# Kernel optimization log

Measured on AMD Instinct MI355X. Metric: run time of the kernel, lower is better.

## Reference

```python
import jax, jax.numpy as jnp
import numpy as np

B, K, L, D, H = 8, 64, 4096, 1024, 16
HD = D // H
SCALE = HD ** -0.5


def setup_inputs() -> dict:
    key = jax.random.key(0)
    ks = jax.random.split(key, 7)
    return {
        "query": jax.random.normal(ks[0], (B, K, D), jnp.float32),
        "key": jax.random.normal(ks[1], (B, L, D), jnp.float32),
        "value": jax.random.normal(ks[2], (B, L, D), jnp.float32),
        "Wq": jax.random.normal(ks[3], (D, D), jnp.float32) * (D ** -0.5),
        "Wk": jax.random.normal(ks[4], (D, D), jnp.float32) * (D ** -0.5),
        "Wv": jax.random.normal(ks[5], (D, D), jnp.float32) * (D ** -0.5),
        "Wo": jax.random.normal(ks[6], (D, D), jnp.float32) * (D ** -0.5),
        "bo": jnp.zeros((D,), jnp.float32),
    }


def reference(query, key, value, Wq, Wk, Wv, Wo, bo):
    # torch Linear: y = x @ W.T; split heads -> [B,H,len,HD]
    q = jnp.einsum('bkd,ed->bke', query, Wq).reshape(B, K, H, HD).transpose(0, 2, 1, 3)
    k = jnp.einsum('bld,ed->ble', key, Wk).reshape(B, L, H, HD).transpose(0, 2, 1, 3)
    v = jnp.einsum('bld,ed->ble', value, Wv).reshape(B, L, H, HD).transpose(0, 2, 1, 3)
    dots = jnp.einsum('bhkc,bhlc->bhkl', q, k) * SCALE  # [B,H,K,L]
    attn = jax.nn.softmax(dots, axis=-2)               # softmax over query (slot) dim
    attn = attn / (attn.sum(axis=-1, keepdims=True) + 1e-8)  # renormalize over keys
    out = jnp.einsum('bhkl,bhlc->bhkc', attn, v)       # [B,H,K,HD]
    out = out.transpose(0, 2, 1, 3).reshape(B, K, D)
    out = jnp.einsum('bkd,ed->bke', out, Wo) + bo
    return out, attn
```

## Files before the change

### kernel.cpp

```cpp
#include <hip/hip_runtime.h>
#include <hip/hip_bf16.h>

#define B_   8
#define KS_  64
#define L_   4096
#define D_   1024
#define H_   16
#define HD_  64
#define SCALE_ 0.125f

typedef __attribute__((ext_vector_type(8))) short short8;
typedef __attribute__((ext_vector_type(8))) unsigned short ushort8;
typedef __attribute__((ext_vector_type(4))) unsigned short ushort4v;
typedef __attribute__((ext_vector_type(4))) float f32x4;

__device__ __forceinline__ unsigned short f2b(float f) {
  union { float f; unsigned u; } v; v.f = f;
  unsigned r = v.u + 0x7fffu + ((v.u >> 16) & 1u);
  return (unsigned short)(r >> 16);
}

typedef const __attribute__((address_space(1))) void gas_void;
typedef __attribute__((address_space(3))) void las_void;
__device__ __forceinline__ void gl2lds16(const void* g, void* l) {
  __builtin_amdgcn_global_load_lds((gas_void*)g, (las_void*)l, 16, 0, 0);
}

__device__ __forceinline__ void bar() {
  asm volatile("" ::: "memory");
  __builtin_amdgcn_s_barrier();
  asm volatile("" ::: "memory");
}
__device__ __forceinline__ void vm4() {
  asm volatile("s_waitcnt vmcnt(4)" ::: "memory");
}

__global__ __launch_bounds__(256) void wcvt(const float* __restrict__ wq,
                                            const float* __restrict__ wk,
                                            const float* __restrict__ wv,
                                            const float* __restrict__ wo,
                                            const float* __restrict__ query,
                                            unsigned short* __restrict__ wout,
                                            unsigned short* __restrict__ qout) {
  int i = blockIdx.x * 256 + threadIdx.x;
  const float* src;
  unsigned short* dst;
  int off;
  if (i < (4 << 18)) {
    int seg = i >> 18;
    off = (i & 0x3ffff) << 2;
    src = (seg == 0) ? wq : (seg == 1) ? wk : (seg == 2) ? wv : wo;
    dst = wout + ((size_t)seg << 20);
  } else {
    off = (i - (4 << 18)) << 2;
    src = query;
    dst = qout;
  }
  f32x4 v = *(const f32x4*)(src + off);
  ushort4v o;
#pragma unroll
  for (int j = 0; j < 4; ++j) o[j] = f2b(v[j]);
  *(ushort4v*)(dst + off) = o;
}

__global__ __launch_bounds__(256) void cvt1(const float* __restrict__ src,
                                            unsigned short* __restrict__ dst,
                                            int nunits) {
  const int stride = gridDim.x * 256;
  for (int i = blockIdx.x * 256 + threadIdx.x; i < nunits; i += stride) {
    const f32x4* p = (const f32x4*)(src + (size_t)i * 8);
    f32x4 a = __builtin_nontemporal_load(p);
    f32x4 b = __builtin_nontemporal_load(p + 1);
    ushort8 o;
#pragma unroll
    for (int j = 0; j < 4; ++j) { o[j] = f2b(a[j]); o[j + 4] = f2b(b[j]); }
    *(ushort8*)(dst + (size_t)i * 8) = o;
  }
}

__global__ __launch_bounds__(512, 2) void gemm256(const unsigned short* __restrict__ A,
                                                  const unsigned short* __restrict__ W,
                                                  unsigned short* __restrict__ C) {
  __shared__ __align__(16) char smem[131072];
  const int tid = threadIdx.x, lane = tid & 63, w = tid >> 6;
  const int g = lane >> 4, c15 = lane & 15;
  const int wm = w >> 2, wn = w & 3;

  const int swz = (blockIdx.x & 7) * 64 + (blockIdx.x >> 3);
  const long m0 = (long)(swz >> 2) * 256;
  const int  n0 = (swz & 3) * 256;

  const int srow = w * 16 + (lane >> 2);
  const int cswz = (lane & 3) ^ ((lane >> 3) & 3);
  const unsigned short* a_sr = A + (m0 + srow) * 1024 + cswz * 8;
  const unsigned short* b_sr = W + (long)(n0 + srow) * 1024 + cswz * 8;
  const int rswz = (g ^ ((c15 >> 1) & 3)) << 4;
  const int aoff = (wm * 128 + c15) * 64 + rswz;
  const int boff = 65536 + (wn * 64 + c15) * 64 + rswz;

  f32x4 acc[8][4] = {};
  short8 af[8], bf[2];

  auto STAGE_A = [&](int d, int kh, int tk) {
    char* dst = smem + d * 32768 + kh * 16384 + w * 1024;
    const unsigned short* src = a_sr + tk * 64 + kh * 32;
    gl2lds16(src,          dst);
    gl2lds16(src + 131072, dst + 8192);
  };
  auto STAGE_B = [&](int d, int kh, int tk) {
    char* dst = smem + 65536 + d * 32768 + kh * 16384 + w * 1024;
    const unsigned short* src = b_sr + tk * 64 + kh * 32;
    gl2lds16(src,          dst);
    gl2lds16(src + 131072, dst + 8192);
  };
  auto LDA = [&](int d, int ks) {
    const char* base = smem + d * 32768 + ks * 16384 + aoff;
#pragma unroll
    for (int m = 0; m < 8; ++m) af[m] = *(const short8*)(base + m * 1024);
  };
  auto LDB = [&](int d, int ks, int nh) {
    const char* base = smem + d * 32768 + ks * 16384 + boff + nh * 2048;
    bf[0] = *(const short8*)(base);
    bf[1] = *(const short8*)(base + 1024);
  };
  auto MM = [&](int nh) {
    __builtin_amdgcn_s_setprio(1);
#pragma unroll
    for (int n2 = 0; n2 < 2; ++n2)
#pragma unroll
      for (int m = 0; m < 8; ++m)
        acc[m][nh * 2 + n2] =
            __builtin_amdgcn_mfma_f32_16x16x32_bf16(af[m], bf[n2], acc[m][nh * 2 + n2], 0, 0, 0);
    __builtin_amdgcn_s_setprio(0);
  };

  STAGE_A(0, 0, 0); STAGE_B(0, 0, 0); STAGE_A(0, 1, 0); STAGE_B(0, 1, 0);
  vm4();
  bar();

#pragma unroll 1
  for (int tk = 0; tk < 16; tk += 2) {
    const bool more = (tk + 2 < 16);
    LDA(0, 0); LDB(0, 0, 0); STAGE_A(1, 0, tk + 1);          bar(); MM(0); bar();
    LDB(0, 0, 1);            STAGE_B(1, 0, tk + 1);  vm4();  bar(); MM(1); bar();
    LDA(0, 1); LDB(0, 1, 0); STAGE_A(1, 1, tk + 1);          bar(); MM(0); bar();
    LDB(0, 1, 1);            STAGE_B(1, 1, tk + 1);  vm4();  bar(); MM(1); bar();
    LDA(1, 0); LDB(1, 0, 0); if (more) STAGE_A(0, 0, tk + 2);        bar(); MM(0); bar();
    LDB(1, 0, 1);            if (more) STAGE_B(0, 0, tk + 2); vm4(); bar(); MM(1); bar();
    LDA(1, 1); LDB(1, 1, 0); if (more) STAGE_A(0, 1, tk + 2);        bar(); MM(0); bar();
    LDB(1, 1, 1);            if (more) STAGE_B(0, 1, tk + 2); vm4(); bar(); MM(1); bar();
  }

  unsigned short* cl = (unsigned short*)smem;
#pragma unroll
  for (int m = 0; m < 8; ++m)
#pragma unroll
    for (int n = 0; n < 4; ++n)
#pragma unroll
      for (int r = 0; r < 4; ++r)
        cl[(wm * 128 + m * 16 + g * 4 + r) * 256 + wn * 64 + n * 16 + c15] =
            f2b(acc[m][n][r]);
  __syncthreads();
  const int row = tid >> 1, half = tid & 1;
  unsigned short*       dst = C + (m0 + row) * 1024 + n0 + half * 128;
  const unsigned short* sl  = cl + row * 256 + half * 128;
#pragma unroll
  for (int i = 0; i < 16; ++i)
    *(ushort8*)(dst + i * 8) = *(const ushort8*)(sl + i * 8);
}

template <bool OUT_F32B>
__global__ __launch_bounds__(256) void gemm_bf16(const unsigned short* __restrict__ A,
                                                 const unsigned short* __restrict__ W,
                                                 void* __restrict__ Cp,
                                                 const float* __restrict__ bias) {
  __shared__ __align__(16) char smem[34816];
  const int tid = threadIdx.x, lane = tid & 63, wv = tid >> 6;
  const int g = lane >> 4, c15 = lane & 15;
  const int wm = wv >> 1, wn = wv & 1;

  const int nwg = gridDim.x;
  const int swz = (blockIdx.x & 7) * (nwg >> 3) + (blockIdx.x >> 3);
  const long m0 = (long)(swz >> 3) * 128;
  const int  n0 = (swz & 7) * 128;

  const int srow = lane >> 2, scol = (lane & 3) * 8;
  const unsigned short* a_src = A + (m0 + srow) * 1024 + scol;
  const unsigned short* b_src = W + (long)(n0 + srow) * 1024 + scol;

  f32x4 acc[4][4] = {};

  auto stage = [&](int buf, int kt) {
    unsigned short* al = (unsigned short*)(smem + buf * 8192);
    unsigned short* bl = (unsigned short*)(smem + 16384 + buf * 8192);
#pragma unroll
    for (int q = 0; q < 2; ++q) {
      const int rbase = q * 64 + wv * 16;
      gl2lds16(a_src + (long)rbase * 1024 + kt * 32, al + rbase * 32);
      gl2lds16(b_src + (long)rbase * 1024 + kt * 32, bl + rbase * 32);
    }
  };

  stage(0, 0);
  __syncthreads();

  int cur = 0;
  for (int kt = 0; kt < 32; ++kt) {
    if (kt + 1 < 32) stage(cur ^ 1, kt + 1);
    const unsigned short* al = (const unsigned short*)(smem + cur * 8192);
    const unsigned short* bl = (const unsigned short*)(smem + 16384 + cur * 8192);
    short8 af[4];
#pragma unroll
    for (int m = 0; m < 4; ++m)
      af[m] = *(const short8*)&al[(wm * 64 + m * 16 + c15) * 32 + g * 8];
#pragma unroll
    for (int n = 0; n < 4; ++n) {
      short8 b8 = *(const short8*)&bl[(wn * 64 + n * 16 + c15) * 32 + g * 8];
#pragma unroll
      for (int m = 0; m < 4; ++m)
        acc[m][n] = __builtin_amdgcn_mfma_f32_16x16x32_bf16(af[m], b8, acc[m][n], 0, 0, 0);
    }
    __syncthreads();
    cur ^= 1;
  }

  if constexpr (OUT_F32B) {
    float* Cf = (float*)Cp;
#pragma unroll
    for (int m = 0; m < 4; ++m)
#pragma unroll
      for (int n = 0; n < 4; ++n)
#pragma unroll
        for (int r = 0; r < 4; ++r) {
          long row = m0 + wm * 64 + m * 16 + g * 4 + r;
          int  col = n0 + wn * 64 + n * 16 + c15;
          Cf[row * 1024 + col] = acc[m][n][r] + bias[col];
        }
  } else {
    unsigned short* c_lds = (unsigned short*)smem;
#pragma unroll
    for (int m = 0; m < 4; ++m)
#pragma unroll
      for (int n = 0; n < 4; ++n)
#pragma unroll
        for (int r = 0; r < 4; ++r)
          c_lds[(wm * 64 + m * 16 + g * 4 + r) * 132 + wn * 64 + n * 16 + c15] =
              f2b(acc[m][n][r]);
    __syncthreads();
    unsigned short* Cb = (unsigned short*)Cp;
    const int row = tid >> 1, half = tid & 1;
    unsigned short*       dst = Cb + (m0 + row) * 1024 + n0 + half * 64;
    const unsigned short* sl  = &c_lds[row * 132 + half * 64];
#pragma unroll
    for (int i = 0; i < 8; ++i)
      *(ushort8*)(dst + i * 8) = *(const ushort8*)(sl + i * 8);
  }
}

__global__ __launch_bounds__(512) void attn_pass1(const unsigned short* __restrict__ q_b,
                                                  const unsigned short* __restrict__ k_b,
                                                  float* __restrict__ rs_part) {
  __shared__ unsigned short q_lds[64][72];
  __shared__ unsigned short k_lds[128][72];
  __shared__ float rs_lds[8][64];
  const int bh = blockIdx.x >> 2, ch = blockIdx.x & 3;
  const int b = bh >> 4, h = bh & 15;
  const int tid = threadIdx.x;
  const int w = tid >> 6, lane = tid & 63;
  const int g = lane >> 4, c15 = lane & 15;

  {
    int slot = tid >> 3, cc = (tid & 7) * 8;
    *(ushort8*)&q_lds[slot][cc] =
        *(const ushort8*)(q_b + (long)(b * 64 + slot) * 1024 + h * 64 + cc);
  }

  float rs[4][4] = {};
  const long kbase = (long)b * L_ * D_ + h * 64;
  const int  sl = tid >> 2, sc = (tid & 3) * 16;

  for (int it = ch * 8; it < ch * 8 + 8; ++it) {
    const int l0 = it * 128;
    ushort8 k0 = *(const ushort8*)(k_b + kbase + (long)(l0 + sl) * 1024 + sc);
    ushort8 k1 = *(const ushort8*)(k_b + kbase + (long)(l0 + sl) * 1024 + sc + 8);
    __syncthreads();
    *(ushort8*)&k_lds[sl][sc]     = k0;
    *(ushort8*)&k_lds[sl][sc + 8] = k1;
    __syncthreads();

    f32x4 s[4] = {};
#pragma unroll
    for (int ks = 0; ks < 2; ++ks) {
      short8 bf = *(const short8*)&k_lds[w * 16 + c15][ks * 32 + g * 8];
#pragma unroll
      for (int m = 0; m < 4; ++m) {
        short8 af = *(const short8*)&q_lds[m * 16 + c15][ks * 32 + g * 8];
        s[m] = __builtin_amdgcn_mfma_f32_16x16x32_bf16(af, bf, s[m], 0, 0, 0);
      }
    }
    float mx = -1e30f;
#pragma unroll
    for (int m = 0; m < 4; ++m)
#pragma unroll
      for (int r = 0; r < 4; ++r) mx = fmaxf(mx, s[m][r]);
    mx = fmaxf(mx, __shfl_xor(mx, 16));
    mx = fmaxf(mx, __shfl_xor(mx, 32));
    float sum = 0.f, p[4][4];
#pragma unroll
    for (int m = 0; m < 4; ++m)
#pragma unroll
      for (int r = 0; r < 4; ++r) { p[m][r] = __expf((s[m][r] - mx) * SCALE_); sum += p[m][r]; }
    sum += __shfl_xor(sum, 16);
    sum += __shfl_xor(sum, 32);
    float rinv = 1.0f / sum;
#pragma unroll
    for (int m = 0; m < 4; ++m)
#pragma unroll
      for (int r = 0; r < 4; ++r) rs[m][r] += p[m][r] * rinv;
  }
#pragma unroll
  for (int m = 0; m < 4; ++m)
#pragma unroll
    for (int r = 0; r < 4; ++r) {
      float v = rs[m][r];
      v += __shfl_xor(v, 1); v += __shfl_xor(v, 2);
      v += __shfl_xor(v, 4); v += __shfl_xor(v, 8);
      if (c15 == 0) rs_lds[w][m * 16 + g * 4 + r] = v;
    }
  __syncthreads();
  if (tid < 64) {
    float t = 0.f;
#pragma unroll
    for (int w2 = 0; w2 < 8; ++w2) t += rs_lds[w2][tid];
    rs_part[(bh * 4 + ch) * 64 + tid] = t;
  }
}

__global__ __launch_bounds__(512) void attn_pass2(const unsigned short* __restrict__ q_b,
                                                  const unsigned short* __restrict__ k_b,
                                                  const unsigned short* __restrict__ v_b,
                                                  const float* __restrict__ rs_part,
                                                  float* __restrict__ attn,
                                                  float* __restrict__ op_part) {
  __shared__ unsigned short q_lds[64][72];
  __shared__ unsigned short k_lds[128][72];
  __shared__ unsigned short vt_lds[64][136];
  __shared__ unsigned short pt_lds[64][136];
  const int bh = blockIdx.x >> 2, ch = blockIdx.x & 3;
  const int b = bh >> 4, h = bh & 15;
  const int tid = threadIdx.x;
  const int w = tid >> 6, lane = tid & 63;
  const int g = lane >> 4, c15 = lane & 15;

  {
    int slot = tid >> 3, cc = (tid & 7) * 8;
    *(ushort8*)&q_lds[slot][cc] =
        *(const ushort8*)(q_b + (long)(b * 64 + slot) * 1024 + h * 64 + cc);
  }

  float inv_r[4][4];
#pragma unroll
  for (int m = 0; m < 4; ++m)
#pragma unroll
    for (int r = 0; r < 4; ++r) {
      int slot = m * 16 + g * 4 + r;
      float s = 0.f;
#pragma unroll
      for (int c = 0; c < 4; ++c) s += rs_part[(bh * 4 + c) * 64 + slot];
      inv_r[m][r] = 1.0f / (s + 1e-8f);
    }

  f32x4 oacc[2] = {};
  const int m_pv = w >> 1, n_pv0 = (w & 1) * 2;
  float* attn_base = attn + (long)bh * KS_ * L_;
  const long base_bld = (long)b * L_ * D_ + h * 64;
  const int  sl = tid >> 2, sc = (tid & 3) * 16;

  for (int it = ch * 8; it < ch * 8 + 8; ++it) {
    const int l0 = it * 128;
    ushort8 k0 = *(const ushort8*)(k_b + base_bld + (long)(l0 + sl) * 1024 + sc);
    ushort8 k1 = *(const ushort8*)(k_b + base_bld + (long)(l0 + sl) * 1024 + sc + 8);
    ushort8 v0 = *(const ushort8*)(v_b + base_bld + (long)(l0 + sl) * 1024 + sc);
    ushort8 v1 = *(const ushort8*)(v_b + base_bld + (long)(l0 + sl) * 1024 + sc + 8);
    __syncthreads();
    *(ushort8*)&k_lds[sl][sc]     = k0;
    *(ushort8*)&k_lds[sl][sc + 8] = k1;
#pragma unroll
    for (int j = 0; j < 8; ++j) {
      vt_lds[sc + j][sl]     = v0[j];
      vt_lds[sc + 8 + j][sl] = v1[j];
    }
    __syncthreads();

    f32x4 s[4] = {};
#pragma unroll
    for (int ks = 0; ks < 2; ++ks) {
      short8 bf = *(const short8*)&k_lds[w * 16 + c15][ks * 32 + g * 8];
#pragma unroll
      for (int m = 0; m < 4; ++m) {
        short8 af = *(const short8*)&q_lds[m * 16 + c15][ks * 32 + g * 8];
        s[m] = __builtin_amdgcn_mfma_f32_16x16x32_bf16(af, bf, s[m], 0, 0, 0);
      }
    }
    float mx = -1e30f;
#pragma unroll
    for (int m = 0; m < 4; ++m)
#pragma unroll
      for (int r = 0; r < 4; ++r) mx = fmaxf(mx, s[m][r]);
    mx = fmaxf(mx, __shfl_xor(mx, 16));
    mx = fmaxf(mx, __shfl_xor(mx, 32));
    float sum = 0.f, p[4][4];
#pragma unroll
    for (int m = 0; m < 4; ++m)
#pragma unroll
      for (int r = 0; r < 4; ++r) { p[m][r] = __expf((s[m][r] - mx) * SCALE_); sum += p[m][r]; }
    sum += __shfl_xor(sum, 16);
    sum += __shfl_xor(sum, 32);
    float rinv = 1.0f / sum;

    const int lloc = w * 16 + c15;
#pragma unroll
    for (int m = 0; m < 4; ++m)
#pragma unroll
      for (int r = 0; r < 4; ++r) {
        float ps = p[m][r] * rinv * inv_r[m][r];
        __builtin_nontemporal_store(ps,
            &attn_base[(long)(m * 16 + g * 4 + r) * L_ + l0 + lloc]);
        pt_lds[m * 16 + g * 4 + r][lloc] = f2b(ps);
      }
    __syncthreads();

#pragma unroll
    for (int ks = 0; ks < 4; ++ks) {
      short8 pa = *(const short8*)&pt_lds[m_pv * 16 + c15][ks * 32 + g * 8];
#pragma unroll
      for (int n2 = 0; n2 < 2; ++n2) {
        short8 vb = *(const short8*)&vt_lds[(n_pv0 + n2) * 16 + c15][ks * 32 + g * 8];
        oacc[n2] = __builtin_amdgcn_mfma_f32_16x16x32_bf16(pa, vb, oacc[n2], 0, 0, 0);
      }
    }
  }

#pragma unroll
  for (int n2 = 0; n2 < 2; ++n2)
#pragma unroll
    for (int r = 0; r < 4; ++r) {
      int slot = m_pv * 16 + g * 4 + r;
      int c    = (n_pv0 + n2) * 16 + c15;
      op_part[((long)(bh * 4 + ch) * 64 + slot) * 64 + c] = oacc[n2][r];
    }
}

__global__ __launch_bounds__(256) void oh_red(const float* __restrict__ op_part,
                                              unsigned short* __restrict__ oh) {
  int i = blockIdx.x * 256 + threadIdx.x;
  int c = i & 63, slot = (i >> 6) & 63, bh = i >> 12;
  float s = 0.f;
#pragma unroll
  for (int ch = 0; ch < 4; ++ch)
    s += op_part[((long)(bh * 4 + ch) * 64 + slot) * 64 + c];
  int b = bh >> 4, h = bh & 15;
  oh[(long)(b * 64 + slot) * 1024 + h * 64 + c] = f2b(s);
}

extern "C" void kernel_launch(void* const* d_in, const int* in_sizes, int n_in,
                              void* d_out, int out_size, void* d_ws, size_t ws_size,
                              hipStream_t stream) {
  (void)in_sizes; (void)n_in; (void)out_size; (void)ws_size;
  const float* query = (const float*)d_in[0];
  const float* key   = (const float*)d_in[1];
  const float* value = (const float*)d_in[2];
  const float* Wq    = (const float*)d_in[3];
  const float* Wk    = (const float*)d_in[4];
  const float* Wv    = (const float*)d_in[5];
  const float* Wo    = (const float*)d_in[6];
  const float* bo    = (const float*)d_in[7];

  char* ws = (char*)d_ws;
  unsigned short* w_all   = (unsigned short*)ws;
  unsigned short* wq_b    = w_all;
  unsigned short* wk_b    = w_all + (1u << 20);
  unsigned short* wv_b    = w_all + (2u << 20);
  unsigned short* wo_b    = w_all + (3u << 20);
  unsigned short* qin_b   = (unsigned short*)(ws + ((size_t)8  << 20));
  unsigned short* q_b     = (unsigned short*)(ws + ((size_t)9  << 20));
  unsigned short* oh_b    = (unsigned short*)(ws + ((size_t)10 << 20));
  float*          rs_part = (float*)         (ws + ((size_t)11 << 20));
  float*          op_part = (float*)         (ws + ((size_t)12 << 20));
  unsigned short* k_b     = (unsigned short*)(ws + ((size_t)20 << 20));
  unsigned short* v_b     = (unsigned short*)(ws + ((size_t)84 << 20));

  float* out  = (float*)d_out;
  float* attn = out + (size_t)B_ * KS_ * D_;

  unsigned short* kin_b = (unsigned short*)attn;
  unsigned short* vin_b = (unsigned short*)attn + ((size_t)32 << 20);

  wcvt<<<4608, 256, 0, stream>>>(Wq, Wk, Wv, Wo, query, w_all, qin_b);
  cvt1<<<4096, 256, 0, stream>>>(key,   kin_b, 4194304);
  cvt1<<<4096, 256, 0, stream>>>(value, vin_b, 4194304);

  gemm_bf16<false><<<32, 256, 0, stream>>>(qin_b, wq_b, q_b, nullptr);
  gemm256<<<512, 512, 0, stream>>>(kin_b, wk_b, k_b);
  gemm256<<<512, 512, 0, stream>>>(vin_b, wv_b, v_b);

  attn_pass1<<<512, 512, 0, stream>>>(q_b, k_b, rs_part);
  attn_pass2<<<512, 512, 0, stream>>>(q_b, k_b, v_b, rs_part, attn, op_part);
  oh_red<<<2048, 256, 0, stream>>>(op_part, oh_b);

  gemm_bf16<true><<<32, 256, 0, stream>>>(oh_b, wo_b, out, bo);
}
```

Baseline: 370.1 us.

## Fuse fp32-to-bf16 key conversion into the K projection GEMM

Adds a GEMM variant that loads fp32 key tiles directly into LDS and converts them to bf16 in registers with packed convert instructions. This removes the separate key conversion pass and its bf16 write and re-read. The new kernel uses a triple-buffered pipeline with 144KB of LDS, which limits it to one workgroup per CU, and it moves twice as many bytes per A tile. The epilogue stores are also rotated per thread so that lanes spread across different column chunks.

```diff
diff --git a/kernel.cpp b/kernel.cpp
--- a/kernel.cpp
+++ b/kernel.cpp
@@ -20,6 +20,12 @@
   return (unsigned short)(r >> 16);
 }
 
+__device__ __forceinline__ unsigned cvtpk(float a, float b) {
+  unsigned r;
+  asm("v_cvt_pk_bf16_f32 %0, %1, %2" : "=v"(r) : "v"(a), "v"(b));
+  return r;
+}
+
 typedef const __attribute__((address_space(1))) void gas_void;
 typedef __attribute__((address_space(3))) void las_void;
 __device__ __forceinline__ void gl2lds16(const void* g, void* l) {
@@ -31,9 +37,9 @@
   __builtin_amdgcn_s_barrier();
   asm volatile("" ::: "memory");
 }
-__device__ __forceinline__ void vm4() {
-  asm volatile("s_waitcnt vmcnt(4)" ::: "memory");
-}
+__device__ __forceinline__ void vm0() { asm volatile("s_waitcnt vmcnt(0)" ::: "memory"); }
+__device__ __forceinline__ void vm4() { asm volatile("s_waitcnt vmcnt(4)" ::: "memory"); }
+__device__ __forceinline__ void vm6() { asm volatile("s_waitcnt vmcnt(6)" ::: "memory"); }
 
 __global__ __launch_bounds__(256) void wcvt(const float* __restrict__ wq,
                                             const float* __restrict__ wk,
@@ -78,6 +84,114 @@
   }
 }
 
+__global__ __launch_bounds__(512) void gemm256f32(const float* __restrict__ A,
+                                                  const unsigned short* __restrict__ W,
+                                                  unsigned short* __restrict__ C) {
+  __shared__ __align__(16) char smem[147456];
+  const int tid = threadIdx.x, lane = tid & 63, w = tid >> 6;
+  const int g = lane >> 4, c15 = lane & 15;
+  const int wm = w >> 2, wn = w & 3;
+
+  const int swz = (blockIdx.x & 7) * 64 + (blockIdx.x >> 3);
+  const long m0 = (long)(swz >> 2) * 256;
+  const int  n0 = (swz & 3) * 256;
+
+  const float* a_sr = A + (m0 + (tid >> 3)) * 1024 + (((tid & 7) ^ ((tid >> 3) & 7)) << 2);
+  const unsigned short* b_sr = W + (long)(n0 + (tid >> 2)) * 1024 + (((tid & 3) ^ ((tid >> 3) & 3)) << 3);
+
+  f32x4 acc[8][4] = {};
+  short8 af[8], bf[2];
+
+  auto SA = [&](int d, int tk, int q) {
+    gl2lds16(a_sr + (long)q * 65536 + tk * 32,
+             smem + d * 32768 + q * 8192 + tid * 16);
+  };
+  auto SB = [&](int d, int tk, int q) {
+    gl2lds16(b_sr + (long)q * 131072 + tk * 32,
+             smem + 98304 + d * 16384 + q * 8192 + tid * 16);
+  };
+  auto LDA = [&](int buf) {
+    const char* ab = smem + buf * 32768;
+    const int c0 = c15 & 7;
+#pragma unroll
+    for (int m = 0; m < 8; ++m) {
+      const char* rb = ab + (wm * 128 + m * 16 + c15) * 128;
+      f32x4 lo = *(const f32x4*)(rb + (((2 * g)     ^ c0) << 4));
+      f32x4 hi = *(const f32x4*)(rb + (((2 * g + 1) ^ c0) << 4));
+      union { unsigned u[4]; short8 s; } t;
+      t.u[0] = cvtpk(lo[0], lo[1]); t.u[1] = cvtpk(lo[2], lo[3]);
+      t.u[2] = cvtpk(hi[0], hi[1]); t.u[3] = cvtpk(hi[2], hi[3]);
+      af[m] = t.s;
+    }
+  };
+  auto LDB1 = [&](int buf, int n) {
+    return *(const short8*)(smem + 98304 + buf * 16384 +
+                            (wn * 64 + n * 16 + c15) * 64 +
+                            ((g ^ ((c15 >> 1) & 3)) << 4));
+  };
+  auto MM = [&](int h) {
+    __builtin_amdgcn_s_setprio(1);
+#pragma unroll
+    for (int n2 = 0; n2 < 2; ++n2)
+#pragma unroll
+      for (int m = 0; m < 8; ++m)
+        acc[m][h * 2 + n2] =
+            __builtin_amdgcn_mfma_f32_16x16x32_bf16(af[m], bf[n2], acc[m][h * 2 + n2], 0, 0, 0);
+    __builtin_amdgcn_s_setprio(0);
+  };
+  auto TILE = [&](int buf, int db, int tk, bool stage, bool drain) {
+    LDA(buf);
+    bf[0] = LDB1(buf, 0); bf[1] = LDB1(buf, 1);
+    if (stage) { SA(db, tk + 2, 0); SA(db, tk + 2, 1); SA(db, tk + 2, 2); }
+    bar(); MM(0); bar();
+    bf[0] = LDB1(buf, 2); bf[1] = LDB1(buf, 3);
+    if (stage) {
+      SA(db, tk + 2, 3); SB(db, tk + 2, 0); SB(db, tk + 2, 1);
+      vm6();
+    } else if (drain) {
+      vm0();
+    }
+    bar(); MM(1); bar();
+  };
+
+#pragma unroll
+  for (int q = 0; q < 4; ++q) SA(0, 0, q);
+  SB(0, 0, 0); SB(0, 0, 1);
+#pragma unroll
+  for (int q = 0; q < 4; ++q) SA(1, 1, q);
+  SB(1, 1, 0); SB(1, 1, 1);
+  vm6();
+  bar();
+
+#pragma unroll 1
+  for (int t = 0; t < 30; t += 3) {
+    TILE(0, 2, t,     true, false);
+    TILE(1, 0, t + 1, true, false);
+    TILE(2, 1, t + 2, true, false);
+  }
+  TILE(0, 2, 30, false, true);
+  TILE(1, 0, 31, false, false);
+
+  unsigned short* cl = (unsigned short*)smem;
+#pragma unroll
+  for (int m = 0; m < 8; ++m)
+#pragma unroll
+    for (int n = 0; n < 4; ++n)
+#pragma unroll
+      for (int r = 0; r < 4; ++r)
+        cl[(wm * 128 + m * 16 + g * 4 + r) * 256 + wn * 64 + n * 16 + c15] =
+            f2b(acc[m][n][r]);
+  __syncthreads();
+  const int row = tid >> 1, half = tid & 1;
+  unsigned short*       dst = C + (m0 + row) * 1024 + n0 + half * 128;
+  const unsigned short* sl  = cl + row * 256 + half * 128;
+#pragma unroll
+  for (int i = 0; i < 16; ++i) {
+    int c = (i + tid) & 15;
+    *(ushort8*)(dst + c * 8) = *(const ushort8*)(sl + c * 8);
+  }
+}
+
 __global__ __launch_bounds__(512, 2) void gemm256(const unsigned short* __restrict__ A,
                                                   const unsigned short* __restrict__ W,
                                                   unsigned short* __restrict__ C) {
@@ -165,8 +279,10 @@
   unsigned short*       dst = C + (m0 + row) * 1024 + n0 + half * 128;
   const unsigned short* sl  = cl + row * 256 + half * 128;
 #pragma unroll
-  for (int i = 0; i < 16; ++i)
-    *(ushort8*)(dst + i * 8) = *(const ushort8*)(sl + i * 8);
+  for (int i = 0; i < 16; ++i) {
+    int c = (i + tid) & 15;
+    *(ushort8*)(dst + c * 8) = *(const ushort8*)(sl + c * 8);
+  }
 }
 
 template <bool OUT_F32B>
@@ -493,16 +609,14 @@
   float* out  = (float*)d_out;
   float* attn = out + (size_t)B_ * KS_ * D_;
 
-  unsigned short* kin_b = (unsigned short*)attn;
-  unsigned short* vin_b = (unsigned short*)attn + ((size_t)32 << 20);
+  unsigned short* vin_b = (unsigned short*)attn;
 
   wcvt<<<4608, 256, 0, stream>>>(Wq, Wk, Wv, Wo, query, w_all, qin_b);
-  cvt1<<<4096, 256, 0, stream>>>(key,   kin_b, 4194304);
   cvt1<<<4096, 256, 0, stream>>>(value, vin_b, 4194304);
 
   gemm_bf16<false><<<32, 256, 0, stream>>>(qin_b, wq_b, q_b, nullptr);
-  gemm256<<<512, 512, 0, stream>>>(kin_b, wk_b, k_b);
-  gemm256<<<512, 512, 0, stream>>>(vin_b, wv_b, v_b);
+  gemm256f32<<<512, 512, 0, stream>>>(key,   wk_b, k_b);
+  gemm256   <<<512, 512, 0, stream>>>(vin_b, wv_b, v_b);
 
   attn_pass1<<<512, 512, 0, stream>>>(q_b, k_b, rs_part);
   attn_pass2<<<512, 512, 0, stream>>>(q_b, k_b, v_b, rs_part, attn, op_part);
```

Measured after the change: 363.3 us. About the same (-1.8%).
